# Kernel optimization log

Hardware: AMD Instinct MI355X
Metric: run time of the kernel (lower is better)

## Reference

```python
import jax, jax.numpy as jnp
import numpy as np

B, N, D = 8, 1024, 512
H = 8
DH = D // H
EPS_DIST = 1e-8
EPS_LN = 1e-5


def _layer_norm(x, gamma, beta):
    mu = jnp.mean(x, axis=-1, keepdims=True)
    var = jnp.mean((x - mu) ** 2, axis=-1, keepdims=True)
    return (x - mu) * jax.lax.rsqrt(var + EPS_LN) * gamma + beta


def setup_inputs() -> dict:
    key = jax.random.key(0)
    ks = jax.random.split(key, 6)
    scale = 1.0 / np.sqrt(D)
    inp = {
        "x": jax.random.normal(ks[0], (B, N, D), dtype=jnp.float32),
        "Wq": jax.random.normal(ks[1], (D, D), dtype=jnp.float32) * scale,
        "Wk": jax.random.normal(ks[2], (D, D), dtype=jnp.float32) * scale,
        "Wv": jax.random.normal(ks[3], (D, D), dtype=jnp.float32) * scale,
        "Wo": jax.random.normal(ks[4], (D, D), dtype=jnp.float32) * scale,
        "bq": jnp.zeros((D,), jnp.float32),
        "bk": jnp.zeros((D,), jnp.float32),
        "bv": jnp.zeros((D,), jnp.float32),
        "bo": jnp.zeros((D,), jnp.float32),
        "ln1_g": jnp.ones((D,), jnp.float32),
        "ln1_b": jnp.zeros((D,), jnp.float32),
        "ln2_g": jnp.ones((D,), jnp.float32),
        "ln2_b": jnp.zeros((D,), jnp.float32),
    }
    return inp


def reference(x, Wq, bq, Wk, bk, Wv, bv, Wo, bo, ln1_g, ln1_b, ln2_g, ln2_b):
    residual = x
    h = _layer_norm(x, ln1_g, ln1_b)  # pre-norm

    def heads(t):
        # [B,N,D] -> [B,H,N,DH]
        return t.reshape(B, N, H, DH).transpose(0, 2, 1, 3)

    q = heads(h @ Wq + bq)
    k = heads(h @ Wk + bk)
    v = heads(h @ Wv + bv)

    # Euclidean pairwise distance via ||q||^2 + ||k||^2 - 2 q.k expansion
    q_sq = jnp.sum(q * q, axis=-1)[..., :, None]      # [B,H,N,1]
    k_sq = jnp.sum(k * k, axis=-1)[..., None, :]      # [B,H,1,N]
    qk = jnp.einsum("bhnd,bhmd->bhnm", q, k)          # [B,H,N,N]
    d2 = jnp.maximum(q_sq + k_sq - 2.0 * qk, 0.0)
    dist = jnp.sqrt(d2 + EPS_DIST)

    # distance -> attention score: smaller distance = higher attention
    attn = jax.nn.softmax(-dist, axis=-1)             # [B,H,N,N]

    out = jnp.einsum("bhnm,bhmd->bhnd", attn, v)      # [B,H,N,DH]
    out = out.transpose(0, 2, 1, 3).reshape(B, N, D)
    out = out @ Wo + bo

    y = residual + out
    y = _layer_norm(y, ln2_g, ln2_b)
    return y
```

## Files before the change

kernel.cpp:

```cpp
#include <hip/hip_runtime.h>
#include <math.h>

typedef __attribute__((ext_vector_type(8))) short short8;
typedef __attribute__((ext_vector_type(4))) float f32x4;
typedef __attribute__((ext_vector_type(2))) unsigned uint2v;

constexpr int B  = 8;
constexpr int N  = 1024;
constexpr int D  = 512;
constexpr int H  = 8;
constexpr int DH = 64;
constexpr int M_ROWS = 8192;
constexpr float EPS_DIST = 1e-8f;
constexpr float EPS_LN   = 1e-5f;

__device__ inline unsigned short bfbits(float f) {
    union { float f; unsigned u; } v; v.f = f;
    unsigned r = v.u + 0x7fffu + ((v.u >> 16) & 1u);
    return (unsigned short)(r >> 16);
}
__device__ inline float bf2f(unsigned short s) {
    union { unsigned u; float f; } v; v.u = ((unsigned)s) << 16; return v.f;
}

__device__ inline void async_ld16(unsigned short* lds, const unsigned short* g) {
    __builtin_amdgcn_global_load_lds(
        (const __attribute__((address_space(1))) unsigned int*)(g),
        (__attribute__((address_space(3))) unsigned int*)(lds),
        16, 0, 0);
}

__global__ __launch_bounds__(256) void prep_kernel(const float* __restrict__ Wq,
                                                   const float* __restrict__ Wk,
                                                   const float* __restrict__ Wv,
                                                   const float* __restrict__ Wo,
                                                   unsigned short* __restrict__ WtAll,
                                                   const float* __restrict__ x,
                                                   const float* __restrict__ ln1_g,
                                                   const float* __restrict__ ln1_b,
                                                   unsigned short* __restrict__ h_bf) {
    const int bxg = blockIdx.x;
    if (bxg < 256) {
        int sub = bxg >> 6;
        const float* W = sub == 0 ? Wq : sub == 1 ? Wk : sub == 2 ? Wv : Wo;
        unsigned short* Wt = WtAll + (size_t)sub * 262144;
        int t = (bxg & 63) * 256 + threadIdx.x;
        int tk = t & 127, tn = t >> 7;
        int k = tk * 4, n = tn * 4;
        float4 r0 = *(const float4*)&W[(size_t)(k + 0) * 512 + n];
        float4 r1 = *(const float4*)&W[(size_t)(k + 1) * 512 + n];
        float4 r2 = *(const float4*)&W[(size_t)(k + 2) * 512 + n];
        float4 r3 = *(const float4*)&W[(size_t)(k + 3) * 512 + n];
        ushort4 c;
        c.x = bfbits(r0.x); c.y = bfbits(r1.x); c.z = bfbits(r2.x); c.w = bfbits(r3.x);
        *(ushort4*)&Wt[(size_t)(n + 0) * 512 + k] = c;
        c.x = bfbits(r0.y); c.y = bfbits(r1.y); c.z = bfbits(r2.y); c.w = bfbits(r3.y);
        *(ushort4*)&Wt[(size_t)(n + 1) * 512 + k] = c;
        c.x = bfbits(r0.z); c.y = bfbits(r1.z); c.z = bfbits(r2.z); c.w = bfbits(r3.z);
        *(ushort4*)&Wt[(size_t)(n + 2) * 512 + k] = c;
        c.x = bfbits(r0.w); c.y = bfbits(r1.w); c.z = bfbits(r2.w); c.w = bfbits(r3.w);
        *(ushort4*)&Wt[(size_t)(n + 3) * 512 + k] = c;
    } else {
        const int w = threadIdx.x >> 6, lane = threadIdx.x & 63;
        const int row = (bxg - 256) * 4 + w;
        const float4* xr = (const float4*)(x + (size_t)row * D);
        float4 a = xr[lane], b2 = xr[lane + 64];
        float s = a.x + a.y + a.z + a.w + b2.x + b2.y + b2.z + b2.w;
        #pragma unroll
        for (int o = 1; o < 64; o <<= 1) s += __shfl_xor(s, o, 64);
        const float mu = s * (1.0f / 512.0f);
        float d0 = a.x - mu, d1 = a.y - mu, d2 = a.z - mu, d3 = a.w - mu;
        float e0 = b2.x - mu, e1 = b2.y - mu, e2 = b2.z - mu, e3 = b2.w - mu;
        float vs = d0*d0 + d1*d1 + d2*d2 + d3*d3 + e0*e0 + e1*e1 + e2*e2 + e3*e3;
        #pragma unroll
        for (int o = 1; o < 64; o <<= 1) vs += __shfl_xor(vs, o, 64);
        const float rstd = rsqrtf(vs * (1.0f / 512.0f) + EPS_LN);
        const float4* g4 = (const float4*)ln1_g;
        const float4* b4 = (const float4*)ln1_b;
        float4 ga = g4[lane], gb = g4[lane + 64];
        float4 ba = b4[lane], bb = b4[lane + 64];
        ushort4 u;
        u.x = bfbits(d0 * rstd * ga.x + ba.x);
        u.y = bfbits(d1 * rstd * ga.y + ba.y);
        u.z = bfbits(d2 * rstd * ga.z + ba.z);
        u.w = bfbits(d3 * rstd * ga.w + ba.w);
        *(ushort4*)&h_bf[(size_t)row * 512 + lane * 4] = u;
        u.x = bfbits(e0 * rstd * gb.x + bb.x);
        u.y = bfbits(e1 * rstd * gb.y + bb.y);
        u.z = bfbits(e2 * rstd * gb.z + bb.z);
        u.w = bfbits(e3 * rstd * gb.w + bb.w);
        *(ushort4*)&h_bf[(size_t)row * 512 + 256 + lane * 4] = u;
    }
}

template <int MODE, int MT>
__global__ __launch_bounds__(256) void gemm128(const unsigned short* __restrict__ A,
                                               const unsigned short* __restrict__ Wt,
                                               const float* __restrict__ bias0,
                                               const float* __restrict__ bias1,
                                               const float* __restrict__ bias2,
                                               void* __restrict__ o0,
                                               unsigned short* __restrict__ Ko,
                                               unsigned short* __restrict__ Vo,
                                               float* __restrict__ sq0,
                                               float* __restrict__ sq1) {
    constexpr int RB = M_ROWS / MT;
    constexpr int NI = MT / 32;
    constexpr int ASZ = MT * 64, BSZ = 128 * 64;
    constexpr int SMSZ = (MODE == 1) ? ((ASZ + BSZ > 18432) ? ASZ + BSZ : 18432)
                                     : (ASZ + BSZ);
    __shared__ unsigned short smem[SMSZ];
    unsigned short* As = smem;
    unsigned short* Bs = smem + ASZ;

    const int id = blockIdx.x;
    const int by = id & (RB - 1), bx = id / RB;
    const int tid = threadIdx.x;
    const int lane = tid & 63, wv = tid >> 6;
    const int quad = lane >> 4, l15 = lane & 15;
    const int row0 = by * MT, col0 = bx * 128;
    const int wm = (wv & 1) * (MT / 2), wn = (wv >> 1) * 64;
    const int fsw = (l15 & 7) << 3;

    f32x4 acc[NI][4];
    #pragma unroll
    for (int i = 0; i < NI; ++i)
        #pragma unroll
        for (int j = 0; j < 4; ++j) acc[i][j] = (f32x4){0.f, 0.f, 0.f, 0.f};

    const unsigned short* Ag = A  + (size_t)row0 * 512;
    const unsigned short* Bg = Wt + (size_t)col0 * 512;

    for (int k0 = 0; k0 < 512; k0 += 64) {
        __syncthreads();
        #pragma unroll
        for (int c = 0; c < ASZ / 2048; ++c) {
            int fu = c * 2048 + tid * 8;
            int r = fu >> 6, ko = fu & 63;
            async_ld16(As + fu, Ag + (size_t)r * 512 + k0 + (ko ^ ((r & 7) << 3)));
        }
        #pragma unroll
        for (int c = 0; c < BSZ / 2048; ++c) {
            int fu = c * 2048 + tid * 8;
            int r = fu >> 6, ko = fu & 63;
            async_ld16(Bs + fu, Bg + (size_t)r * 512 + k0 + (ko ^ ((r & 7) << 3)));
        }
        __syncthreads();

        #pragma unroll
        for (int ks = 0; ks < 2; ++ks) {
            short8 af[NI], bf[4];
            #pragma unroll
            for (int i = 0; i < NI; ++i)
                af[i] = *(const short8*)&As[(wm + i * 16 + l15) * 64 +
                                            ((ks * 32 + quad * 8) ^ fsw)];
            #pragma unroll
            for (int j = 0; j < 4; ++j)
                bf[j] = *(const short8*)&Bs[(wn + j * 16 + l15) * 64 +
                                            ((ks * 32 + quad * 8) ^ fsw)];
            #pragma unroll
            for (int i = 0; i < NI; ++i)
                #pragma unroll
                for (int j = 0; j < 4; ++j)
                    acc[i][j] = __builtin_amdgcn_mfma_f32_16x16x32_bf16(af[i], bf[j], acc[i][j], 0, 0, 0);
        }
    }

    if (MODE == 0) {
        unsigned short* C = (unsigned short*)o0;
        #pragma unroll
        for (int i = 0; i < NI; ++i)
            #pragma unroll
            for (int j = 0; j < 4; ++j) {
                int col = col0 + wn + j * 16 + l15;
                float bv = bias0[col];
                #pragma unroll
                for (int r = 0; r < 4; ++r) {
                    int row = row0 + wm + i * 16 + quad * 4 + r;
                    C[(size_t)row * 512 + col] = bfbits(acc[i][j][r] + bv);
                }
            }
    } else {
        const int colg = col0 + wn;
        const int seg = colg >> 9;
        const int hh = (colg & 511) >> 6;
        const float* bias = seg == 0 ? bias0 : seg == 1 ? bias1 : bias2;

        __syncthreads();
        unsigned short* T = smem + wv * 4608;

        if (seg < 2) {
            unsigned short* dst = seg == 0 ? (unsigned short*)o0 : Ko;
            float* sq = seg == 0 ? sq0 : sq1;
            #pragma unroll
            for (int i = 0; i < NI; ++i) {
                const int m0 = row0 + wm + i * 16 + quad * 4;
                float ss[4] = {0.f, 0.f, 0.f, 0.f};
                #pragma unroll
                for (int j = 0; j < 4; ++j) {
                    float bvj = bias[hh * 64 + j * 16 + l15];
                    #pragma unroll
                    for (int r = 0; r < 4; ++r) {
                        float v = acc[i][j][r] + bvj;
                        unsigned short ub = bfbits(v);
                        float vr = bf2f(ub);
                        ss[r] += vr * vr;
                        T[(i * 16 + quad * 4 + r) * 72 + j * 16 + l15] = ub;
                    }
                }
                #pragma unroll
                for (int r = 0; r < 4; ++r) {
                    float s = ss[r];
                    s += __shfl_xor(s, 1, 64);
                    s += __shfl_xor(s, 2, 64);
                    s += __shfl_xor(s, 4, 64);
                    s += __shfl_xor(s, 8, 64);
                    if (l15 == 0) {
                        int m = m0 + r;
                        sq[(size_t)((m >> 10) * 8 + hh) * 1024 + (m & 1023)] = s;
                    }
                }
            }
            const int b_ = (row0 + wm) >> 10;
            const int nbase = (row0 + wm) & 1023;
            unsigned short* Dg = dst + ((size_t)((b_ * 8 + hh) * 1024 + nbase)) * 64;
            #pragma unroll
            for (int it = 0; it < 8; ++it) {
                int ml = it * 8 + (lane >> 3);
                int dl = (lane & 7) * 8;
                uint4 v = *(const uint4*)&T[ml * 72 + dl];
                *(uint4*)&Dg[(size_t)ml * 64 + dl] = v;
            }
        } else {
            #pragma unroll
            for (int i = 0; i < NI; ++i)
                #pragma unroll
                for (int j = 0; j < 4; ++j) {
                    float bvj = bias[hh * 64 + j * 16 + l15];
                    ushort4 pk;
                    pk.x = bfbits(acc[i][j][0] + bvj);
                    pk.y = bfbits(acc[i][j][1] + bvj);
                    pk.z = bfbits(acc[i][j][2] + bvj);
                    pk.w = bfbits(acc[i][j][3] + bvj);
                    *(ushort4*)&T[(j * 16 + l15) * 72 + i * 16 + quad * 4] = pk;
                }
            const int b_ = (row0 + wm) >> 10;
            const int nbase = (row0 + wm) & 1023;
            unsigned short* Vg = Vo + ((size_t)((b_ * 8 + hh) * 64)) * 1024 + nbase;
            #pragma unroll
            for (int it = 0; it < 8; ++it) {
                int dl = it * 8 + (lane >> 3);
                int nl = (lane & 7) * 8;
                uint4 v = *(const uint4*)&T[dl * 72 + nl];
                *(uint4*)&Vg[(size_t)dl * 1024 + nl] = v;
            }
        }
    }
}

__global__ __launch_bounds__(256) void projln_kernel(const unsigned short* __restrict__ A,
                                                     const unsigned short* __restrict__ Wt,
                                                     const float* __restrict__ bo,
                                                     const float* __restrict__ x,
                                                     const float* __restrict__ gamma,
                                                     const float* __restrict__ beta,
                                                     float* __restrict__ out) {
    __shared__ unsigned short smem[2048 + 32768];
    __shared__ float st[128];
    unsigned short* As = smem;
    unsigned short* Bs = smem + 2048;

    const int tid = threadIdx.x;
    const int lane = tid & 63, w = tid >> 6;
    const int quad = lane >> 4, l15 = lane & 15;
    const int rows0 = blockIdx.x * 32;
    const int fsw = (l15 & 7) << 3;

    f32x4 acc[2][8];
    #pragma unroll
    for (int i = 0; i < 2; ++i)
        #pragma unroll
        for (int j = 0; j < 8; ++j) acc[i][j] = (f32x4){0.f, 0.f, 0.f, 0.f};

    const unsigned short* Ag = A + (size_t)rows0 * 512;
    const int sr = tid >> 3;
    const int sko = (tid & 7) * 8;

    for (int k0 = 0; k0 < 512; k0 += 64) {
        __syncthreads();
        async_ld16(As + tid * 8,
                   Ag + (size_t)sr * 512 + k0 + (sko ^ ((sr & 7) << 3)));
        #pragma unroll
        for (int c = 0; c < 16; ++c) {
            int fu = c * 2048 + tid * 8;
            int r = c * 32 + sr;
            async_ld16(Bs + fu,
                       Wt + (size_t)r * 512 + k0 + (sko ^ ((r & 7) << 3)));
        }
        __syncthreads();

        #pragma unroll
        for (int ks = 0; ks < 2; ++ks) {
            short8 af[2], bf[8];
            #pragma unroll
            for (int i = 0; i < 2; ++i)
                af[i] = *(const short8*)&As[(i * 16 + l15) * 64 +
                                            ((ks * 32 + quad * 8) ^ fsw)];
            #pragma unroll
            for (int j = 0; j < 8; ++j)
                bf[j] = *(const short8*)&Bs[(w * 128 + j * 16 + l15) * 64 +
                                            ((ks * 32 + quad * 8) ^ fsw)];
            #pragma unroll
            for (int i = 0; i < 2; ++i)
                #pragma unroll
                for (int j = 0; j < 8; ++j)
                    acc[i][j] = __builtin_amdgcn_mfma_f32_16x16x32_bf16(af[i], bf[j], acc[i][j], 0, 0, 0);
        }
    }

    float s1[2][4] = {{0.f, 0.f, 0.f, 0.f}, {0.f, 0.f, 0.f, 0.f}};
    #pragma unroll
    for (int i = 0; i < 2; ++i)
        #pragma unroll
        for (int j = 0; j < 8; ++j) {
            const int colj = w * 128 + j * 16 + l15;
            const float bvj = bo[colj];
            #pragma unroll
            for (int r = 0; r < 4; ++r) {
                const int row = i * 16 + quad * 4 + r;
                float y = acc[i][j][r] + bvj +
                          x[(size_t)(rows0 + row) * 512 + colj];
                acc[i][j][r] = y;
                s1[i][r] += y;
            }
        }
    #pragma unroll
    for (int i = 0; i < 2; ++i)
        #pragma unroll
        for (int r = 0; r < 4; ++r) {
            s1[i][r] += __shfl_xor(s1[i][r], 1, 64);
            s1[i][r] += __shfl_xor(s1[i][r], 2, 64);
            s1[i][r] += __shfl_xor(s1[i][r], 4, 64);
            s1[i][r] += __shfl_xor(s1[i][r], 8, 64);
        }
    if (l15 == 0) {
        #pragma unroll
        for (int i = 0; i < 2; ++i)
            #pragma unroll
            for (int r = 0; r < 4; ++r)
                st[w * 32 + i * 16 + quad * 4 + r] = s1[i][r];
    }
    __syncthreads();
    float mu[2][4];
    #pragma unroll
    for (int i = 0; i < 2; ++i)
        #pragma unroll
        for (int r = 0; r < 4; ++r) {
            int row = i * 16 + quad * 4 + r;
            mu[i][r] = (st[row] + st[32 + row] + st[64 + row] + st[96 + row]) *
                       (1.0f / 512.0f);
        }
    __syncthreads();

    float s2[2][4] = {{0.f, 0.f, 0.f, 0.f}, {0.f, 0.f, 0.f, 0.f}};
    #pragma unroll
    for (int i = 0; i < 2; ++i)
        #pragma unroll
        for (int j = 0; j < 8; ++j)
            #pragma unroll
            for (int r = 0; r < 4; ++r) {
                float d = acc[i][j][r] - mu[i][r];
                s2[i][r] += d * d;
            }
    #pragma unroll
    for (int i = 0; i < 2; ++i)
        #pragma unroll
        for (int r = 0; r < 4; ++r) {
            s2[i][r] += __shfl_xor(s2[i][r], 1, 64);
            s2[i][r] += __shfl_xor(s2[i][r], 2, 64);
            s2[i][r] += __shfl_xor(s2[i][r], 4, 64);
            s2[i][r] += __shfl_xor(s2[i][r], 8, 64);
        }
    if (l15 == 0) {
        #pragma unroll
        for (int i = 0; i < 2; ++i)
            #pragma unroll
            for (int r = 0; r < 4; ++r)
                st[w * 32 + i * 16 + quad * 4 + r] = s2[i][r];
    }
    __syncthreads();
    float rs[2][4];
    #pragma unroll
    for (int i = 0; i < 2; ++i)
        #pragma unroll
        for (int r = 0; r < 4; ++r) {
            int row = i * 16 + quad * 4 + r;
            float var = (st[row] + st[32 + row] + st[64 + row] + st[96 + row]) *
                        (1.0f / 512.0f);
            rs[i][r] = rsqrtf(var + EPS_LN);
        }

    #pragma unroll
    for (int i = 0; i < 2; ++i)
        #pragma unroll
        for (int j = 0; j < 8; ++j) {
            const int colj = w * 128 + j * 16 + l15;
            const float gl = gamma[colj], bl = beta[colj];
            #pragma unroll
            for (int r = 0; r < 4; ++r) {
                const int row = i * 16 + quad * 4 + r;
                out[(size_t)(rows0 + row) * 512 + colj] =
                    (acc[i][j][r] - mu[i][r]) * rs[i][r] * gl + bl;
            }
        }
}

__global__ __launch_bounds__(256, 2) void attn_kernel(const unsigned short* __restrict__ Q,
                                                      const unsigned short* __restrict__ K,
                                                      const unsigned short* __restrict__ Vt,
                                                      const float* __restrict__ qsq,
                                                      const float* __restrict__ ksq,
                                                      unsigned short* __restrict__ O) {
    __shared__ unsigned short smem[2 * 4096 + 2 * 4096 + 256];
    unsigned short* KsB = smem;
    unsigned short* VsB = smem + 8192;
    float* ksq_s = (float*)(smem + 16384);

    const int id = blockIdx.x;
    const int bh = id & 63, qb = id >> 6;
    const int q0 = qb * 128;
    const int tid = threadIdx.x;
    const int lane = tid & 63, w = tid >> 6;
    const int quad = lane >> 4, l15 = lane & 15;
    const int b_ = bh >> 3, h_ = bh & 7;

    const unsigned short* Qb = Q  + (size_t)bh * N * DH;
    const unsigned short* Kb = K  + (size_t)bh * N * DH;
    const unsigned short* Vb = Vt + (size_t)bh * DH * N;

    short8 qf[2][2];
    #pragma unroll
    for (int qh = 0; qh < 2; ++qh) {
        const unsigned short* qp = Qb + (size_t)(q0 + w * 32 + qh * 16 + l15) * 64 + quad * 8;
        qf[qh][0] = *(const short8*)qp;
        qf[qh][1] = *(const short8*)(qp + 32);
        unsigned* qw = (unsigned*)&qf[qh][0];
        #pragma unroll
        for (int j = 0; j < 8; ++j) qw[j] = (qw[j] ^ 0x80008000u) + 0x00800080u;
    }
    float qe[2];
    qe[0] = qsq[bh * N + q0 + w * 32 + l15] + EPS_DIST;
    qe[1] = qsq[bh * N + q0 + w * 32 + 16 + l15] + EPS_DIST;

    const short8 onesf = {0x3F80, 0x3F80, 0x3F80, 0x3F80, 0x3F80, 0x3F80, 0x3F80, 0x3F80};

    f32x4 oacc[2][4];
    f32x4 dsum[2];
    #pragma unroll
    for (int qh = 0; qh < 2; ++qh) {
        dsum[qh] = (f32x4){0.f, 0.f, 0.f, 0.f};
        #pragma unroll
        for (int dt = 0; dt < 4; ++dt) oacc[qh][dt] = (f32x4){0.f, 0.f, 0.f, 0.f};
    }

    const int srow = tid >> 3;
    const int scol = ((tid & 7) * 8) ^ ((srow & 7) << 3);

    #pragma unroll
    for (int c = 0; c < 2; ++c) {
        const int e = c * 2048 + tid * 8;
        const int row = srow + c * 32;
        async_ld16(KsB + e, Kb + (size_t)row * 64 + scol);
        async_ld16(VsB + e, Vb + (size_t)row * N + scol);
    }
    if (tid < 64) ksq_s[tid] = ksq[bh * N + tid];
    __syncthreads();

    for (int kt = 0; kt < 16; ++kt) {
        const int cur = kt & 1;
        float ksreg = 0.f;
        if (kt < 15) {
            const int t64 = (kt + 1) * 64;
            #pragma unroll
            for (int c = 0; c < 2; ++c) {
                const int e = (cur ^ 1) * 4096 + c * 2048 + tid * 8;
                const int row = srow + c * 32;
                const int cg = ((tid & 7) * 8) ^ ((row & 7) << 3);
                async_ld16(KsB + e, Kb + (size_t)(t64 + row) * 64 + cg);
                async_ld16(VsB + e, Vb + (size_t)row * N + t64 + cg);
            }
            if (tid < 64) ksreg = ksq[bh * N + t64 + tid];
        }

        #pragma unroll
        for (int kc = 0; kc < 2; ++kc) {
            unsigned Wp[2][2][2];
            #pragma unroll
            for (int kh = 0; kh < 2; ++kh) {
                const int kb = kc * 2 + kh;
                const int krow = kb * 16 + l15;
                const int ksw = (krow & 7) << 3;
                const unsigned short* kbase = KsB + cur * 4096 + krow * 64;
                short8 kf0 = *(const short8*)&kbase[(quad * 8) ^ ksw];
                short8 kf1 = *(const short8*)&kbase[(32 + quad * 8) ^ ksw];
                f32x4 ks2 = *(const f32x4*)&ksq_s[cur * 64 + kb * 16 + quad * 4];
                #pragma unroll
                for (int qh = 0; qh < 2; ++qh) {
                    f32x4 sa;
                    #pragma unroll
                    for (int r = 0; r < 4; ++r) sa[r] = ks2[r] + qe[qh];
                    sa = __builtin_amdgcn_mfma_f32_16x16x32_bf16(kf0, qf[qh][0], sa, 0, 0, 0);
                    sa = __builtin_amdgcn_mfma_f32_16x16x32_bf16(kf1, qf[qh][1], sa, 0, 0, 0);
                    float pr[4];
                    #pragma unroll
                    for (int r = 0; r < 4; ++r) {
                        float d2 = fmaxf(sa[r], EPS_DIST);
                        pr[r] = __expf(-__builtin_amdgcn_sqrtf(d2));
                    }
                    union { float f; unsigned u; } u0, u1, u2, u3;
                    u0.f = pr[0]; u1.f = pr[1]; u2.f = pr[2]; u3.f = pr[3];
                    Wp[qh][kh][0] = __builtin_amdgcn_perm(u1.u, u0.u, 0x07060302u);
                    Wp[qh][kh][1] = __builtin_amdgcn_perm(u3.u, u2.u, 0x07060302u);
                }
            }

            short8 vf[4];
            #pragma unroll
            for (int dt = 0; dt < 4; ++dt) {
                const int vrow = dt * 16 + l15;
                vf[dt] = *(const short8*)&VsB[cur * 4096 + vrow * 64 +
                                              ((kc * 32 + quad * 8) ^ ((vrow & 7) << 3))];
            }

            #pragma unroll
            for (int qh = 0; qh < 2; ++qh) {
                uint2v ya = __builtin_amdgcn_permlane32_swap(Wp[qh][0][0], Wp[qh][1][0], false, false);
                uint2v za = __builtin_amdgcn_permlane16_swap(ya.x, ya.y, false, false);
                uint2v yb = __builtin_amdgcn_permlane32_swap(Wp[qh][0][1], Wp[qh][1][1], false, false);
                uint2v zb = __builtin_amdgcn_permlane16_swap(yb.x, yb.y, false, false);
                union { unsigned wds[4]; short8 s; } pu;
                pu.wds[0] = za.x; pu.wds[1] = zb.x; pu.wds[2] = za.y; pu.wds[3] = zb.y;
                short8 pf = pu.s;
                dsum[qh] = __builtin_amdgcn_mfma_f32_16x16x32_bf16(pf, onesf, dsum[qh], 0, 0, 0);
                #pragma unroll
                for (int dt = 0; dt < 4; ++dt)
                    oacc[qh][dt] = __builtin_amdgcn_mfma_f32_16x16x32_bf16(pf, vf[dt], oacc[qh][dt], 0, 0, 0);
            }
        }

        if (kt < 15 && tid < 64) ksq_s[(cur ^ 1) * 64 + tid] = ksreg;
        __syncthreads();
    }

    unsigned short* T3 = smem + w * 2304;
    #pragma unroll
    for (int qh = 0; qh < 2; ++qh) {
        f32x4 rv;
        #pragma unroll
        for (int r = 0; r < 4; ++r) rv[r] = __builtin_amdgcn_rcpf(dsum[qh][r]);
        #pragma unroll
        for (int dt = 0; dt < 4; ++dt)
            #pragma unroll
            for (int r = 0; r < 4; ++r)
                T3[(qh * 16 + quad * 4 + r) * 72 + dt * 16 + l15] =
                    bfbits(oacc[qh][dt][r] * rv[r]);
    }
    unsigned short* Og = O + ((size_t)(b_ * N + q0 + w * 32) * D) + h_ * DH;
    #pragma unroll
    for (int it = 0; it < 4; ++it) {
        int ml = it * 8 + (lane >> 3);
        int dl = (lane & 7) * 8;
        uint4 v = *(const uint4*)&T3[ml * 72 + dl];
        *(uint4*)&Og[(size_t)ml * D + dl] = v;
    }
}

extern "C" void kernel_launch(void* const* d_in, const int* in_sizes, int n_in,
                              void* d_out, int out_size, void* d_ws, size_t ws_size,
                              hipStream_t stream) {
    const float* x     = (const float*)d_in[0];
    const float* Wq    = (const float*)d_in[1];
    const float* Wk    = (const float*)d_in[2];
    const float* Wv    = (const float*)d_in[3];
    const float* Wo    = (const float*)d_in[4];
    const float* bq    = (const float*)d_in[5];
    const float* bk    = (const float*)d_in[6];
    const float* bv    = (const float*)d_in[7];
    const float* bo    = (const float*)d_in[8];
    const float* ln1_g = (const float*)d_in[9];
    const float* ln1_b = (const float*)d_in[10];
    const float* ln2_g = (const float*)d_in[11];
    const float* ln2_b = (const float*)d_in[12];
    float* out = (float*)d_out;

    unsigned short* WtAll = (unsigned short*)d_ws;
    unsigned short* h_bf  = WtAll + 4 * 262144;
    unsigned short* Qb    = h_bf + 4194304;
    unsigned short* Kb    = Qb + 4194304;
    unsigned short* Vtg   = Kb + 4194304;
    unsigned short* Ob    = Vtg + 4194304;
    float* qsq = (float*)(Ob + 4194304);
    float* ksq = qsq + 65536;

    prep_kernel<<<256 + M_ROWS / 4, 256, 0, stream>>>(Wq, Wk, Wv, Wo, WtAll,
                                                      x, ln1_g, ln1_b, h_bf);

    gemm128<1, 128><<<768, 256, 0, stream>>>(h_bf, WtAll, bq, bk, bv,
                                             Qb, Kb, Vtg, qsq, ksq);

    attn_kernel<<<512, 256, 0, stream>>>(Qb, Kb, Vtg, qsq, ksq, Ob);

    projln_kernel<<<256, 256, 0, stream>>>(Ob, WtAll + 3 * 262144, bo,
                                           x, ln2_g, ln2_b, out);
}
```

Before: 171.4 us.

## Load K/V fragments directly from global memory, dropping LDS staging and barriers

The attention kernel no longer stages K, V and ksq tiles into double-buffered shared memory with async loads and per-tile barriers. Each wave now reads its MFMA operand fragments straight from global memory and relies on L1/L2 caching, with the key loop unrolled by 2. This removes LDS traffic and block-wide synchronisation, but each of the four waves now fetches the same K/V data separately. Global loads are uncoalesced row fragments, so latency hiding depends on the compiler and on occupancy.

```diff
diff --git a/kernel.cpp b/kernel.cpp
--- a/kernel.cpp
+++ b/kernel.cpp
@@ -421,10 +421,7 @@
                                                       const float* __restrict__ qsq,
                                                       const float* __restrict__ ksq,
                                                       unsigned short* __restrict__ O) {
-    __shared__ unsigned short smem[2 * 4096 + 2 * 4096 + 256];
-    unsigned short* KsB = smem;
-    unsigned short* VsB = smem + 8192;
-    float* ksq_s = (float*)(smem + 16384);
+    __shared__ unsigned short T3all[4][2304];
 
     const int id = blockIdx.x;
     const int bh = id & 63, qb = id >> 6;
@@ -437,6 +434,7 @@
     const unsigned short* Qb = Q  + (size_t)bh * N * DH;
     const unsigned short* Kb = K  + (size_t)bh * N * DH;
     const unsigned short* Vb = Vt + (size_t)bh * DH * N;
+    const float* ksb = ksq + (size_t)bh * N;
 
     short8 qf[2][2];
     #pragma unroll
@@ -463,47 +461,19 @@
         for (int dt = 0; dt < 4; ++dt) oacc[qh][dt] = (f32x4){0.f, 0.f, 0.f, 0.f};
     }
 
-    const int srow = tid >> 3;
-    const int scol = ((tid & 7) * 8) ^ ((srow & 7) << 3);
-
-    #pragma unroll
-    for (int c = 0; c < 2; ++c) {
-        const int e = c * 2048 + tid * 8;
-        const int row = srow + c * 32;
-        async_ld16(KsB + e, Kb + (size_t)row * 64 + scol);
-        async_ld16(VsB + e, Vb + (size_t)row * N + scol);
-    }
-    if (tid < 64) ksq_s[tid] = ksq[bh * N + tid];
-    __syncthreads();
-
+    #pragma unroll 2
     for (int kt = 0; kt < 16; ++kt) {
-        const int cur = kt & 1;
-        float ksreg = 0.f;
-        if (kt < 15) {
-            const int t64 = (kt + 1) * 64;
-            #pragma unroll
-            for (int c = 0; c < 2; ++c) {
-                const int e = (cur ^ 1) * 4096 + c * 2048 + tid * 8;
-                const int row = srow + c * 32;
-                const int cg = ((tid & 7) * 8) ^ ((row & 7) << 3);
-                async_ld16(KsB + e, Kb + (size_t)(t64 + row) * 64 + cg);
-                async_ld16(VsB + e, Vb + (size_t)row * N + t64 + cg);
-            }
-            if (tid < 64) ksreg = ksq[bh * N + t64 + tid];
-        }
-
+        const int k0 = kt * 64;
         #pragma unroll
         for (int kc = 0; kc < 2; ++kc) {
             unsigned Wp[2][2][2];
             #pragma unroll
             for (int kh = 0; kh < 2; ++kh) {
                 const int kb = kc * 2 + kh;
-                const int krow = kb * 16 + l15;
-                const int ksw = (krow & 7) << 3;
-                const unsigned short* kbase = KsB + cur * 4096 + krow * 64;
-                short8 kf0 = *(const short8*)&kbase[(quad * 8) ^ ksw];
-                short8 kf1 = *(const short8*)&kbase[(32 + quad * 8) ^ ksw];
-                f32x4 ks2 = *(const f32x4*)&ksq_s[cur * 64 + kb * 16 + quad * 4];
+                const unsigned short* kp = Kb + (size_t)(k0 + kb * 16 + l15) * 64 + quad * 8;
+                short8 kf0 = *(const short8*)kp;
+                short8 kf1 = *(const short8*)(kp + 32);
+                f32x4 ks2 = *(const f32x4*)&ksb[k0 + kb * 16 + quad * 4];
                 #pragma unroll
                 for (int qh = 0; qh < 2; ++qh) {
                     f32x4 sa;
@@ -526,11 +496,9 @@
 
             short8 vf[4];
             #pragma unroll
-            for (int dt = 0; dt < 4; ++dt) {
-                const int vrow = dt * 16 + l15;
-                vf[dt] = *(const short8*)&VsB[cur * 4096 + vrow * 64 +
-                                              ((kc * 32 + quad * 8) ^ ((vrow & 7) << 3))];
-            }
+            for (int dt = 0; dt < 4; ++dt)
+                vf[dt] = *(const short8*)&Vb[(size_t)(dt * 16 + l15) * N +
+                                             k0 + kc * 32 + quad * 8];
 
             #pragma unroll
             for (int qh = 0; qh < 2; ++qh) {
@@ -547,12 +515,9 @@
                     oacc[qh][dt] = __builtin_amdgcn_mfma_f32_16x16x32_bf16(pf, vf[dt], oacc[qh][dt], 0, 0, 0);
             }
         }
-
-        if (kt < 15 && tid < 64) ksq_s[(cur ^ 1) * 64 + tid] = ksreg;
-        __syncthreads();
-    }
-
-    unsigned short* T3 = smem + w * 2304;
+    }
+
+    unsigned short* T3 = &T3all[w][0];
     #pragma unroll
     for (int qh = 0; qh < 2; ++qh) {
         f32x4 rv;
```

Measured after the change: 203.0 us. 1.18x slower.
